# Optimization experiments

Measured on AMD Instinct MI355X. Metric: run time of the kernel, lower is better.

Reference implementation:

```python
import jax, jax.numpy as jnp
import numpy as np

HIDDEN = 1024
NUM_HEADS = 4
HEAD_DIM = HIDDEN // NUM_HEADS
SCALE = HEAD_DIM ** -0.5
EPS = 1e-5


def setup_inputs() -> dict:
    key = jax.random.key(0)
    ks = jax.random.split(key, 8)
    B, S, D = 4, 2048, HIDDEN
    x = jax.random.normal(ks[0], (B, S, D), dtype=jnp.float32)
    attention_mask = jnp.ones((B, S), dtype=jnp.int32)
    init = 1.0 / np.sqrt(D)
    Wq = jax.random.uniform(ks[1], (D, D), jnp.float32, -init, init)
    Wk = jax.random.uniform(ks[2], (D, D), jnp.float32, -init, init)
    Wv = jax.random.uniform(ks[3], (D, D), jnp.float32, -init, init)
    Wo = jax.random.uniform(ks[4], (D, D), jnp.float32, -init, init)
    bo = jax.random.uniform(ks[5], (D,), jnp.float32, -init, init)
    gamma = jnp.ones((D,), dtype=jnp.float32)
    beta = jnp.zeros((D,), dtype=jnp.float32)
    return {"x": x, "attention_mask": attention_mask, "Wq": Wq, "Wk": Wk,
            "Wv": Wv, "Wo": Wo, "bo": bo, "gamma": gamma, "beta": beta}


def reference(x, attention_mask, Wq, Wk, Wv, Wo, bo, gamma, beta):
    # Linear layers: y = x @ W^T (torch nn.Linear convention), no bias for q/k/v
    q = jnp.einsum('bsd,ed->bse', x, Wq)
    k = jnp.einsum('bsd,ed->bse', x, Wk)
    v = jnp.einsum('bsd,ed->bse', x, Wv)
    # Full-width attention (module never splits heads), scale = head_dim^-0.5
    scores = jnp.einsum('bqd,bkd->bqk', q, k) * SCALE  # [B,S,S]
    mask = attention_mask[:, None, :]  # [B,1,S]
    scores = jnp.where(mask == 0, jnp.float32(-1e9), scores)
    attn = jax.nn.softmax(scores, axis=-1)
    ctx = jnp.einsum('bqk,bkd->bqd', attn, v)
    out = jnp.einsum('bsd,ed->bse', ctx, Wo) + bo
    # residual + LayerNorm
    h = out + x
    mu = jnp.mean(h, axis=-1, keepdims=True)
    var = jnp.mean(jnp.square(h - mu), axis=-1, keepdims=True)
    return (h - mu) * jax.lax.rsqrt(var + EPS) * gamma + beta
```

## Files before the change

### kernel.cpp

```cpp
#include <hip/hip_runtime.h>

typedef __bf16 bf16;
typedef __bf16 bf16x8 __attribute__((ext_vector_type(8)));
typedef __bf16 bf16x4 __attribute__((ext_vector_type(4)));
typedef float floatx4 __attribute__((ext_vector_type(4)));

#define HIDDEN 1024
#define SEQ 2048
#define BATCH 4
#define ATT_SCALE 0.0625f
#define LN_EPS 1e-5f
#define WW (HIDDEN * HIDDEN)

__device__ __forceinline__ void gload_lds16(const void* g, void* l) {
    __builtin_amdgcn_global_load_lds(
        (const __attribute__((address_space(1))) unsigned int*)g,
        (__attribute__((address_space(3))) unsigned int*)l, 16, 0, 0);
}

#define GBAR() asm volatile("s_barrier" ::: "memory")
#define LGKM0() asm volatile("s_waitcnt lgkmcnt(0)" ::: "memory")
#define VMC(N) asm volatile("s_waitcnt vmcnt(" #N ")" ::: "memory")
#define MFMA(a, b, c) __builtin_amdgcn_mfma_f32_16x16x32_bf16(a, b, c, 0, 0, 0)
#define MFMA8(a, b, c) __builtin_amdgcn_mfma_f32_16x16x32_fp8_fp8(a, b, c, 0, 0, 0)

__device__ __forceinline__ unsigned char to_fp8(float f) {
    return (unsigned char)(__builtin_amdgcn_cvt_pk_fp8_f32(f, 0.0f, 0, 0) & 0xff);
}
__device__ __forceinline__ unsigned int to_fp8x2(float a, float b) {
    return __builtin_amdgcn_cvt_pk_fp8_f32(a, b, 0, 0) & 0xffff;
}

__global__ void cvt_f32_bf16(const float* __restrict__ in, bf16* __restrict__ out, int n4) {
    int i = blockIdx.x * blockDim.x + threadIdx.x;
    if (i >= n4) return;
    float4 v = ((const float4*)in)[i];
    bf16x4 o;
    o[0] = (bf16)v.x; o[1] = (bf16)v.y; o[2] = (bf16)v.z; o[3] = (bf16)v.w;
    ((bf16x4*)out)[i] = o;
}

__global__ void cvt_f32_fp8(const float* __restrict__ in, unsigned char* __restrict__ out, int n8) {
    int i = blockIdx.x * blockDim.x + threadIdx.x;
    if (i >= n8) return;
    float4 v0 = ((const float4*)in)[i * 2];
    float4 v1 = ((const float4*)in)[i * 2 + 1];
    unsigned int lo = to_fp8x2(v0.x, v0.y) | (to_fp8x2(v0.z, v0.w) << 16);
    unsigned int hi = to_fp8x2(v1.x, v1.y) | (to_fp8x2(v1.z, v1.w) << 16);
    ((uint2*)out)[i] = make_uint2(lo, hi);
}

__global__ void transpose_w3(const float* __restrict__ s0, const float* __restrict__ s1,
                             const float* __restrict__ s2,
                             bf16* __restrict__ d0p, bf16* __restrict__ d1p, bf16* __restrict__ d2p) {
    const float* in = (blockIdx.z == 0) ? s0 : (blockIdx.z == 1) ? s1 : s2;
    bf16* out = (blockIdx.z == 0) ? d0p : (blockIdx.z == 1) ? d1p : d2p;
    __shared__ __attribute__((aligned(16))) bf16 tile[64][72];
    const int d0 = blockIdx.x * 64;
    const int f0 = blockIdx.y * 64;
    const int t = threadIdx.x;
    const int r = t >> 4;
    const int c = (t & 15) * 4;
#pragma unroll
    for (int i = 0; i < 4; ++i) {
        float4 v = *(const float4*)&in[(long)(f0 + r + i * 16) * HIDDEN + d0 + c];
        bf16x4 b;
        b[0] = (bf16)v.x; b[1] = (bf16)v.y; b[2] = (bf16)v.z; b[3] = (bf16)v.w;
        *(bf16x4*)&tile[r + i * 16][c] = b;
    }
    __syncthreads();
#pragma unroll
    for (int i = 0; i < 4; ++i) {
        const int dr = r + i * 16;
        bf16x4 o;
#pragma unroll
        for (int j = 0; j < 4; ++j) o[j] = tile[c + j][dr];
        *(bf16x4*)&out[(long)(d0 + dr) * HIDDEN + f0 + c] = o;
    }
}

template <int MODE>
__global__ __launch_bounds__(512, 2)
void gemm8p(const bf16* A, const bf16* Bw, void* __restrict__ Cout,
            int lda, int ldb, int ldc, int K, float scale,
            long sA, long sB, long sC, int zmod) {
    __shared__ __attribute__((aligned(16))) char lds[131072];

    const int gx = gridDim.x;
    const int nblk = gx * gridDim.y;
    const int bid = blockIdx.y * gx + blockIdx.x;
    const int cpx = nblk >> 3;
    const int sbid = (nblk & 7) ? bid : (bid & 7) * cpx + (bid >> 3);
    const int bx = sbid % gx, by = sbid / gx;

    const int z = blockIdx.z;
    const int mat = z % zmod, ks = z / zmod;
    const char* Ab = (const char*)(A + (long)mat * sA + (long)ks * K);
    const char* Bb = (const char*)(Bw + (long)mat * sB + (long)ks * K);
    const long lda2 = lda * 2L, ldb2 = ldb * 2L;

    const int t = threadIdx.x;
    const int lane = t & 63;
    const int w = t >> 6;
    const int wm = w >> 2;
    const int wn = w & 3;
    const int l15 = lane & 15;
    const int l4 = lane >> 4;

    const int row0 = by * 256;
    const int col0 = bx * 256;

    const int sc = ((((t & 3) - ((t >> 3) & 3)) & 3) << 4);
    const char* aS[2];
    const char* bS[2];
#pragma unroll
    for (int uu = 0; uu < 2; ++uu) {
        aS[uu] = Ab + (long)(row0 + uu * 128 + (t >> 2)) * lda2 + sc;
        bS[uu] = Bb + (long)(col0 + uu * 128 + (t >> 2)) * ldb2 + sc;
    }

    auto STAGE = [&](char* dstu, const char* const* sp, long koff) {
        gload_lds16(sp[0] + koff, dstu + t * 16);
        gload_lds16(sp[1] + koff, dstu + 8192 + t * 16);
    };

    floatx4 acc[8][4] = {};
    const int nk = K / 64;

    STAGE(lds + 0,     aS, 0);
    STAGE(lds + 16384, bS, 0);
    STAGE(lds + 32768, aS, 64);
    STAGE(lds + 49152, bS, 64);
    VMC(4);
    GBAR();

    for (int tt = 0; tt < nk; ++tt) {
        const char* cb = lds + (tt & 1) * 65536;
        char* nb = lds + ((tt & 1) ^ 1) * 65536;
        const long nko = (long)((tt + 1 < nk) ? tt + 1 : nk - 1) * 128;

        auto RDA = [&](int kk, int m) {
            int lr = wm * 128 + m * 16 + l15;
            return *(const bf16x8*)(cb + kk * 32768 + lr * 64 + ((((lr >> 1) + l4) & 3) << 4));
        };
        auto RDB = [&](int kk, int n) {
            int lr = wn * 64 + n * 16 + l15;
            return *(const bf16x8*)(cb + 16384 + kk * 32768 + lr * 64 + ((((lr >> 1) + l4) & 3) << 4));
        };

        bf16x8 a[4], b0[4], b1[4];

#pragma unroll
        for (int m = 0; m < 4; ++m) a[m] = RDA(0, m);
#pragma unroll
        for (int n = 0; n < 4; ++n) b0[n] = RDB(0, n);
        STAGE(nb + 0, aS, nko);
        GBAR();
        LGKM0();
        __builtin_amdgcn_s_setprio(1);
#pragma unroll
        for (int m = 0; m < 4; ++m)
#pragma unroll
            for (int n = 0; n < 4; ++n) acc[m][n] = MFMA(a[m], b0[n], acc[m][n]);
        __builtin_amdgcn_s_setprio(0);
        GBAR();

#pragma unroll
        for (int m = 0; m < 4; ++m) a[m] = RDA(0, 4 + m);
        STAGE(nb + 16384, bS, nko);
        GBAR();
        LGKM0();
        __builtin_amdgcn_s_setprio(1);
#pragma unroll
        for (int m = 0; m < 4; ++m)
#pragma unroll
            for (int n = 0; n < 4; ++n) acc[4 + m][n] = MFMA(a[m], b0[n], acc[4 + m][n]);
        __builtin_amdgcn_s_setprio(0);
        VMC(4);
        GBAR();

#pragma unroll
        for (int m = 0; m < 4; ++m) a[m] = RDA(1, m);
#pragma unroll
        for (int n = 0; n < 4; ++n) b1[n] = RDB(1, n);
        STAGE(nb + 32768, aS, nko + 64);
        GBAR();
        LGKM0();
        __builtin_amdgcn_s_setprio(1);
#pragma unroll
        for (int m = 0; m < 4; ++m)
#pragma unroll
            for (int n = 0; n < 4; ++n) acc[m][n] = MFMA(a[m], b1[n], acc[m][n]);
        __builtin_amdgcn_s_setprio(0);
        GBAR();

#pragma unroll
        for (int m = 0; m < 4; ++m) a[m] = RDA(1, 4 + m);
        STAGE(nb + 49152, bS, nko + 64);
        GBAR();
        LGKM0();
        __builtin_amdgcn_s_setprio(1);
#pragma unroll
        for (int m = 0; m < 4; ++m)
#pragma unroll
            for (int n = 0; n < 4; ++n) acc[4 + m][n] = MFMA(a[m], b1[n], acc[4 + m][n]);
        __builtin_amdgcn_s_setprio(0);
        VMC(4);
        GBAR();
    }
    VMC(0);

    const int rq = l4 * 4;
    if constexpr (MODE == 0) {
        bf16* C = ((bf16*)Cout) + (long)z * sC;
#pragma unroll
        for (int m = 0; m < 8; ++m)
#pragma unroll
            for (int i = 0; i < 4; ++i) {
                long gr = row0 + wm * 128 + m * 16 + rq + i;
#pragma unroll
                for (int n = 0; n < 4; ++n) {
                    int gc = col0 + wn * 64 + n * 16 + l15;
                    C[gr * ldc + gc] = (bf16)(acc[m][n][i] * scale);
                }
            }
    } else {
        float* C = (float*)Cout + (long)z * sC;
#pragma unroll
        for (int m = 0; m < 8; ++m)
#pragma unroll
            for (int i = 0; i < 4; ++i) {
                long gr = row0 + wm * 128 + m * 16 + rq + i;
#pragma unroll
                for (int n = 0; n < 4; ++n) {
                    int gc = col0 + wn * 64 + n * 16 + l15;
                    C[gr * ldc + gc] = acc[m][n][i];
                }
            }
    }
}

template <int MODE>
__global__ __launch_bounds__(512, 2)
void gemmf8(const unsigned char* A, const unsigned char* Bw, void* __restrict__ Cout,
            int lda, int ldb, int ldc, int K, float scale,
            long sA, long sB, long sC, int zmod) {
    __shared__ __attribute__((aligned(16))) char lds[65536];

    const int gx = gridDim.x;
    const int nblk = gx * gridDim.y;
    const int bid = blockIdx.y * gx + blockIdx.x;
    const int cpx = nblk >> 3;
    const int sbid = (nblk & 7) ? bid : (bid & 7) * cpx + (bid >> 3);
    const int bx = sbid % gx, by = sbid / gx;

    const int z = blockIdx.z;
    const int mat = z % zmod, ks = z / zmod;
    const unsigned char* Ab = A + (long)mat * sA + (long)ks * K;
    const unsigned char* Bb = Bw + (long)mat * sB + (long)ks * K;

    const int t = threadIdx.x;
    const int lane = t & 63;
    const int w = t >> 6;
    const int wm = w >> 2;
    const int wn = w & 3;
    const int l15 = lane & 15;
    const int l4 = lane >> 4;

    const int row0 = by * 256;
    const int col0 = bx * 256;

    const int r_st = t >> 1;
    const int u_g = ((t & 1) + (t >> 3)) & 1;
    const unsigned char* aSrc = Ab + (long)(row0 + r_st) * lda + u_g * 16;
    const unsigned char* bSrc = Bb + (long)(col0 + r_st) * ldb + u_g * 16;
    const int ld16 = t * 16;

    auto STAGE = [&](int slot, long koff) {
        char* base = lds + slot * 32768;
        gload_lds16(aSrc + koff,      base + ld16);
        gload_lds16(aSrc + koff + 32, base + 8192 + ld16);
        gload_lds16(bSrc + koff,      base + 16384 + ld16);
        gload_lds16(bSrc + koff + 32, base + 24576 + ld16);
    };

    floatx4 acc[8][4] = {};
    const int nk = K / 64;

    STAGE(0, 0);
    VMC(0);
    GBAR();

    for (int s = 0; s < nk; ++s) {
        const char* sb = lds + (s & 1) * 32768;
        const long pko = (long)((s + 1 < nk) ? s + 1 : nk - 1) * 64;
        STAGE((s + 1) & 1, pko);

        auto RD = [&](const char* unit, int r) {
            int addr = r * 32 + ((((l4 >> 1) + (r >> 2)) & 1) << 4) + ((l4 & 1) << 3);
            return *(const long*)(unit + addr);
        };

        long a[8], b[4];
#pragma unroll
        for (int n = 0; n < 4; ++n) b[n] = RD(sb + 16384, wn * 64 + n * 16 + l15);
#pragma unroll
        for (int m = 0; m < 8; ++m) a[m] = RD(sb, wm * 128 + m * 16 + l15);
        __builtin_amdgcn_s_setprio(1);
#pragma unroll
        for (int m = 0; m < 8; ++m)
#pragma unroll
            for (int n = 0; n < 4; ++n) acc[m][n] = MFMA8(a[m], b[n], acc[m][n]);
        __builtin_amdgcn_s_setprio(0);
#pragma unroll
        for (int n = 0; n < 4; ++n) b[n] = RD(sb + 24576, wn * 64 + n * 16 + l15);
#pragma unroll
        for (int m = 0; m < 8; ++m) a[m] = RD(sb + 8192, wm * 128 + m * 16 + l15);
        __builtin_amdgcn_s_setprio(1);
#pragma unroll
        for (int m = 0; m < 8; ++m)
#pragma unroll
            for (int n = 0; n < 4; ++n) acc[m][n] = MFMA8(a[m], b[n], acc[m][n]);
        __builtin_amdgcn_s_setprio(0);

        VMC(0);
        GBAR();
    }

    const int rq = l4 * 4;
    if constexpr (MODE == 0) {
        bf16* C = ((bf16*)Cout) + (long)z * sC;
#pragma unroll
        for (int m = 0; m < 8; ++m)
#pragma unroll
            for (int i = 0; i < 4; ++i) {
                long gr = row0 + wm * 128 + m * 16 + rq + i;
#pragma unroll
                for (int n = 0; n < 4; ++n) {
                    int gc = col0 + wn * 64 + n * 16 + l15;
                    C[gr * ldc + gc] = (bf16)(acc[m][n][i] * scale);
                }
            }
    } else {
        unsigned char* C = ((unsigned char*)Cout) + (long)z * sC;
#pragma unroll
        for (int m = 0; m < 8; ++m)
#pragma unroll
            for (int i = 0; i < 4; ++i) {
                long gr = row0 + wm * 128 + m * 16 + rq + i;
#pragma unroll
                for (int n = 0; n < 4; ++n) {
                    int gc = col0 + wn * 64 + n * 16 + l15;
                    C[gr * ldc + gc] = to_fp8(acc[m][n][i] * scale);
                }
            }
    }
}

__global__ void reduce_wgc(const float* __restrict__ p, unsigned char* __restrict__ out) {
    int i = blockIdx.x * blockDim.x + threadIdx.x;
    int e = i * 4;
    int mat = e >> 20;
    int local = e & (WW - 1);
    float4 s = *(const float4*)(p + (long)mat * WW + local);
#pragma unroll
    for (int ksp = 1; ksp < 4; ++ksp) {
        float4 a = *(const float4*)(p + (long)(ksp * 2 + mat) * WW + local);
        s.x += a.x; s.y += a.y; s.z += a.z; s.w += a.w;
    }
    unsigned int pk = to_fp8x2(s.x * 64.f, s.y * 64.f) | (to_fp8x2(s.z * 64.f, s.w * 64.f) << 16);
    *(unsigned int*)&out[e] = pk;
}

__global__ void softmax_rows(const bf16* __restrict__ S, unsigned char* __restrict__ P,
                             const int* __restrict__ mask) {
    const int b = blockIdx.y;
    const int row = blockIdx.x;
    const bf16* srow = S + ((long)b * SEQ + row) * SEQ;
    unsigned char* prow = P + ((long)b * SEQ + row) * SEQ;
    const int* mrow = mask + b * SEQ;
    const int t = threadIdx.x;

    bf16x8 sv = *(const bf16x8*)&srow[t * 8];
    int4 m0 = ((const int4*)mrow)[t * 2];
    int4 m1 = ((const int4*)mrow)[t * 2 + 1];
    int mk[8] = {m0.x, m0.y, m0.z, m0.w, m1.x, m1.y, m1.z, m1.w};

    float v[8];
    float mx = -1e30f;
#pragma unroll
    for (int j = 0; j < 8; ++j) {
        float s = (float)sv[j];
        if (mk[j] == 0) s = -1e9f;
        v[j] = s;
        mx = fmaxf(mx, s);
    }
    __shared__ float redm[4], reds[4];
#pragma unroll
    for (int off = 32; off > 0; off >>= 1) mx = fmaxf(mx, __shfl_down(mx, off));
    if ((t & 63) == 0) redm[t >> 6] = mx;
    __syncthreads();
    mx = fmaxf(fmaxf(redm[0], redm[1]), fmaxf(redm[2], redm[3]));

    float sum = 0.f;
#pragma unroll
    for (int j = 0; j < 8; ++j) {
        v[j] = __expf(v[j] - mx);
        sum += v[j];
    }
#pragma unroll
    for (int off = 32; off > 0; off >>= 1) sum += __shfl_down(sum, off);
    if ((t & 63) == 0) reds[t >> 6] = sum;
    __syncthreads();
    sum = reds[0] + reds[1] + reds[2] + reds[3];
    float inv = 256.0f / sum;

    unsigned int lo = to_fp8x2(v[0] * inv, v[1] * inv) | (to_fp8x2(v[2] * inv, v[3] * inv) << 16);
    unsigned int hi = to_fp8x2(v[4] * inv, v[5] * inv) | (to_fp8x2(v[6] * inv, v[7] * inv) << 16);
    *(uint2*)&prow[t * 8] = make_uint2(lo, hi);
}

__global__ void transpose_v8(const unsigned char* __restrict__ yv, unsigned char* __restrict__ out) {
    __shared__ unsigned char tile[64][68];
    const int z = blockIdx.z;
    const unsigned char* ib = yv + (long)z * SEQ * 2048 + 1024;
    unsigned char* ob = out + (long)z * (long)HIDDEN * SEQ;
    const int d0 = blockIdx.x * 64;
    const int s0 = blockIdx.y * 64;
    const int t = threadIdx.x;
    const int r = t >> 4;
    const int c = (t & 15) * 4;
#pragma unroll
    for (int i = 0; i < 4; ++i) {
        uchar4 v = *(const uchar4*)&ib[(long)(s0 + r + i * 16) * 2048 + d0 + c];
        *(uchar4*)&tile[r + i * 16][c] = v;
    }
    __syncthreads();
#pragma unroll
    for (int i = 0; i < 4; ++i) {
        const int dr = r + i * 16;
        uchar4 o;
        o.x = tile[c + 0][dr]; o.y = tile[c + 1][dr];
        o.z = tile[c + 2][dr]; o.w = tile[c + 3][dr];
        *(uchar4*)&ob[(long)(d0 + dr) * SEQ + s0 + c] = o;
    }
}

__global__ void layernorm_out(const bf16* __restrict__ pp, const float* __restrict__ x,
                              const float* __restrict__ bo, const float* __restrict__ gamma,
                              const float* __restrict__ beta, float* __restrict__ out) {
    const long row = blockIdx.x;
    const int b = (int)(row >> 11);
    const int s = (int)(row & 2047);
    const bf16* r0 = pp + ((long)b * SEQ + s) * HIDDEN;
    const bf16* r1 = r0 + 4L * SEQ * HIDDEN;
    const int t = threadIdx.x;

    bf16x4 a0 = ((const bf16x4*)r0)[t];
    bf16x4 a1 = ((const bf16x4*)r1)[t];
    float4 xv = ((const float4*)(x + row * HIDDEN))[t];
    float4 bv = ((const float4*)bo)[t];
    float4 v;
    v.x = (float)a0[0] + (float)a1[0] + bv.x + xv.x;
    v.y = (float)a0[1] + (float)a1[1] + bv.y + xv.y;
    v.z = (float)a0[2] + (float)a1[2] + bv.z + xv.z;
    v.w = (float)a0[3] + (float)a1[3] + bv.w + xv.w;

    float ssum = v.x + v.y + v.z + v.w;
    float sq = v.x * v.x + v.y * v.y + v.z * v.z + v.w * v.w;
    __shared__ float rs[4], rq[4];
#pragma unroll
    for (int off = 32; off > 0; off >>= 1) {
        ssum += __shfl_down(ssum, off);
        sq += __shfl_down(sq, off);
    }
    if ((t & 63) == 0) { rs[t >> 6] = ssum; rq[t >> 6] = sq; }
    __syncthreads();
    ssum = rs[0] + rs[1] + rs[2] + rs[3];
    sq = rq[0] + rq[1] + rq[2] + rq[3];
    float mu = ssum * (1.0f / HIDDEN);
    float var = sq * (1.0f / HIDDEN) - mu * mu;
    float rinv = rsqrtf(var + LN_EPS);
    float4 g = ((const float4*)gamma)[t];
    float4 bt = ((const float4*)beta)[t];
    float4 o;
    o.x = (v.x - mu) * rinv * g.x + bt.x;
    o.y = (v.y - mu) * rinv * g.y + bt.y;
    o.z = (v.z - mu) * rinv * g.z + bt.z;
    o.w = (v.w - mu) * rinv * g.w + bt.w;
    ((float4*)(out + row * HIDDEN))[t] = o;
}

extern "C" void kernel_launch(void* const* d_in, const int* in_sizes, int n_in,
                              void* d_out, int out_size, void* d_ws, size_t ws_size,
                              hipStream_t stream) {
    const float* x     = (const float*)d_in[0];
    const int*   mask  = (const int*)d_in[1];
    const float* Wq    = (const float*)d_in[2];
    const float* Wk    = (const float*)d_in[3];
    const float* Wv    = (const float*)d_in[4];
    const float* Wo    = (const float*)d_in[5];
    const float* bo    = (const float*)d_in[6];
    const float* gamma = (const float*)d_in[7];
    const float* beta  = (const float*)d_in[8];
    float* out = (float*)d_out;

    char* ws = (char*)d_ws;
    const long MB = 1024L * 1024L;
    unsigned char* xb8  = (unsigned char*)(ws + 0 * MB);
    unsigned char* yv8  = (unsigned char*)(ws + 8 * MB);
    unsigned char* vt8  = (unsigned char*)(ws + 24 * MB);
    unsigned char* wgc8 = (unsigned char*)(ws + 32 * MB);
    bf16* wkT = (bf16*)(ws + 34 * MB);
    bf16* wo  = (bf16*)(ws + 36 * MB);
    bf16* wqT = (bf16*)(ws + 38 * MB);
    bf16* wvT = (bf16*)(ws + 40 * MB);
    bf16* S   = (bf16*)(ws + 42 * MB);
    float* wgcp = (float*)(ws + 42 * MB);
    bf16* pp  = (bf16*)(ws + 42 * MB);
    unsigned char* P8 = (unsigned char*)(ws + 74 * MB);

    const int BS = BATCH * SEQ;
    dim3 blk256(256), blk512(512);

    cvt_f32_fp8<<<dim3(BS * HIDDEN / 8 / 256), blk256, 0, stream>>>(x, xb8, BS * HIDDEN / 8);
    cvt_f32_bf16<<<dim3(WW / 4 / 256), blk256, 0, stream>>>(Wo, wo, WW / 4);
    transpose_w3<<<dim3(16, 16, 3), blk256, 0, stream>>>(Wq, Wk, Wv, wqT, wkT, wvT);

    gemm8p<4><<<dim3(1024 / 256, 1024 / 256, 8), blk512, 0, stream>>>(
        wkT, wqT, wgcp, HIDDEN, HIDDEN, HIDDEN, 256, 1.0f,
        (long)WW, (long)WW, (long)WW, 2);
    reduce_wgc<<<dim3(2 * WW / 4 / 256), blk256, 0, stream>>>(wgcp, wgc8);

    gemmf8<1><<<dim3(2048 / 256, BS / 256, 1), blk512, 0, stream>>>(
        xb8, wgc8, yv8, HIDDEN, HIDDEN, 2048, HIDDEN, 1.0f / 64.0f, 0, 0, 0, 1);

    transpose_v8<<<dim3(HIDDEN / 64, SEQ / 64, BATCH), blk256, 0, stream>>>(yv8, vt8);

    gemmf8<0><<<dim3(SEQ / 256, SEQ / 256, BATCH), blk512, 0, stream>>>(
        yv8, xb8, S, 2048, HIDDEN, SEQ, HIDDEN, ATT_SCALE,
        (long)SEQ * 2048, (long)SEQ * HIDDEN, (long)SEQ * SEQ, 4);

    softmax_rows<<<dim3(SEQ, BATCH), blk256, 0, stream>>>(S, P8, mask);

    gemmf8<0><<<dim3(HIDDEN / 256, SEQ / 256, 8), blk512, 0, stream>>>(
        P8, vt8, pp, SEQ, SEQ, HIDDEN, 1024, 1.0f / 256.0f,
        (long)SEQ * SEQ, (long)HIDDEN * SEQ, (long)SEQ * HIDDEN, 4);

    layernorm_out<<<dim3(BS), blk256, 0, stream>>>(pp, x, bo, gamma, beta, out);
}
```

Baseline: 169.7 us.

## Shrink fp8 GEMM tiles to 256x128 with 4 waves; fuse weight prep; bf16 partials

```diff
diff --git a/kernel.cpp b/kernel.cpp
--- a/kernel.cpp
+++ b/kernel.cpp
@@ -29,15 +29,6 @@
 }
 __device__ __forceinline__ unsigned int to_fp8x2(float a, float b) {
     return __builtin_amdgcn_cvt_pk_fp8_f32(a, b, 0, 0) & 0xffff;
-}
-
-__global__ void cvt_f32_bf16(const float* __restrict__ in, bf16* __restrict__ out, int n4) {
-    int i = blockIdx.x * blockDim.x + threadIdx.x;
-    if (i >= n4) return;
-    float4 v = ((const float4*)in)[i];
-    bf16x4 o;
-    o[0] = (bf16)v.x; o[1] = (bf16)v.y; o[2] = (bf16)v.z; o[3] = (bf16)v.w;
-    ((bf16x4*)out)[i] = o;
 }
 
 __global__ void cvt_f32_fp8(const float* __restrict__ in, unsigned char* __restrict__ out, int n8) {
@@ -50,17 +41,29 @@
     ((uint2*)out)[i] = make_uint2(lo, hi);
 }
 
-__global__ void transpose_w3(const float* __restrict__ s0, const float* __restrict__ s1,
-                             const float* __restrict__ s2,
-                             bf16* __restrict__ d0p, bf16* __restrict__ d1p, bf16* __restrict__ d2p) {
-    const float* in = (blockIdx.z == 0) ? s0 : (blockIdx.z == 1) ? s1 : s2;
-    bf16* out = (blockIdx.z == 0) ? d0p : (blockIdx.z == 1) ? d1p : d2p;
-    __shared__ __attribute__((aligned(16))) bf16 tile[64][72];
+__global__ void transpose_w4(const float* __restrict__ s0, const float* __restrict__ s1,
+                             const float* __restrict__ s2, const float* __restrict__ s3,
+                             bf16* __restrict__ d0p, bf16* __restrict__ d1p,
+                             bf16* __restrict__ d2p, bf16* __restrict__ d3p) {
+    const int zz = blockIdx.z;
+    const float* in = (zz == 0) ? s0 : (zz == 1) ? s1 : (zz == 2) ? s2 : s3;
+    bf16* out = (zz == 0) ? d0p : (zz == 1) ? d1p : (zz == 2) ? d2p : d3p;
     const int d0 = blockIdx.x * 64;
     const int f0 = blockIdx.y * 64;
     const int t = threadIdx.x;
     const int r = t >> 4;
     const int c = (t & 15) * 4;
+    if (zz == 3) {
+#pragma unroll
+        for (int i = 0; i < 4; ++i) {
+            float4 v = *(const float4*)&in[(long)(f0 + r + i * 16) * HIDDEN + d0 + c];
+            bf16x4 b;
+            b[0] = (bf16)v.x; b[1] = (bf16)v.y; b[2] = (bf16)v.z; b[3] = (bf16)v.w;
+            *(bf16x4*)&out[(long)(f0 + r + i * 16) * HIDDEN + d0 + c] = b;
+        }
+        return;
+    }
+    __shared__ __attribute__((aligned(16))) bf16 tile[64][72];
 #pragma unroll
     for (int i = 0; i < 4; ++i) {
         float4 v = *(const float4*)&in[(long)(f0 + r + i * 16) * HIDDEN + d0 + c];
@@ -211,41 +214,26 @@
     VMC(0);
 
     const int rq = l4 * 4;
-    if constexpr (MODE == 0) {
-        bf16* C = ((bf16*)Cout) + (long)z * sC;
-#pragma unroll
-        for (int m = 0; m < 8; ++m)
-#pragma unroll
-            for (int i = 0; i < 4; ++i) {
-                long gr = row0 + wm * 128 + m * 16 + rq + i;
-#pragma unroll
-                for (int n = 0; n < 4; ++n) {
-                    int gc = col0 + wn * 64 + n * 16 + l15;
-                    C[gr * ldc + gc] = (bf16)(acc[m][n][i] * scale);
-                }
+    bf16* C = ((bf16*)Cout) + (long)z * sC;
+#pragma unroll
+    for (int m = 0; m < 8; ++m)
+#pragma unroll
+        for (int i = 0; i < 4; ++i) {
+            long gr = row0 + wm * 128 + m * 16 + rq + i;
+#pragma unroll
+            for (int n = 0; n < 4; ++n) {
+                int gc = col0 + wn * 64 + n * 16 + l15;
+                C[gr * ldc + gc] = (bf16)(acc[m][n][i] * scale);
             }
-    } else {
-        float* C = (float*)Cout + (long)z * sC;
-#pragma unroll
-        for (int m = 0; m < 8; ++m)
-#pragma unroll
-            for (int i = 0; i < 4; ++i) {
-                long gr = row0 + wm * 128 + m * 16 + rq + i;
-#pragma unroll
-                for (int n = 0; n < 4; ++n) {
-                    int gc = col0 + wn * 64 + n * 16 + l15;
-                    C[gr * ldc + gc] = acc[m][n][i];
-                }
-            }
-    }
+        }
 }
 
 template <int MODE>
-__global__ __launch_bounds__(512, 2)
+__global__ __launch_bounds__(256, 3)
 void gemmf8(const unsigned char* A, const unsigned char* Bw, void* __restrict__ Cout,
             int lda, int ldb, int ldc, int K, float scale,
             long sA, long sB, long sC, int zmod) {
-    __shared__ __attribute__((aligned(16))) char lds[65536];
+    __shared__ __attribute__((aligned(16))) char lds[49152];
 
     const int gx = gridDim.x;
     const int nblk = gx * gridDim.y;
@@ -262,26 +250,29 @@
     const int t = threadIdx.x;
     const int lane = t & 63;
     const int w = t >> 6;
-    const int wm = w >> 2;
-    const int wn = w & 3;
+    const int wm = w >> 1;
+    const int wn = w & 1;
     const int l15 = lane & 15;
     const int l4 = lane >> 4;
 
     const int row0 = by * 256;
-    const int col0 = bx * 256;
+    const int col0 = bx * 128;
 
     const int r_st = t >> 1;
     const int u_g = ((t & 1) + (t >> 3)) & 1;
-    const unsigned char* aSrc = Ab + (long)(row0 + r_st) * lda + u_g * 16;
-    const unsigned char* bSrc = Bb + (long)(col0 + r_st) * ldb + u_g * 16;
+    const unsigned char* aS0 = Ab + (long)(row0 + r_st) * lda + u_g * 16;
+    const unsigned char* aS1 = Ab + (long)(row0 + 128 + r_st) * lda + u_g * 16;
+    const unsigned char* bS0 = Bb + (long)(col0 + r_st) * ldb + u_g * 16;
     const int ld16 = t * 16;
 
     auto STAGE = [&](int slot, long koff) {
-        char* base = lds + slot * 32768;
-        gload_lds16(aSrc + koff,      base + ld16);
-        gload_lds16(aSrc + koff + 32, base + 8192 + ld16);
-        gload_lds16(bSrc + koff,      base + 16384 + ld16);
-        gload_lds16(bSrc + koff + 32, base + 24576 + ld16);
+        char* base = lds + slot * 24576;
+        gload_lds16(aS0 + koff,      base + ld16);
+        gload_lds16(aS1 + koff,      base + 4096 + ld16);
+        gload_lds16(aS0 + koff + 32, base + 8192 + ld16);
+        gload_lds16(aS1 + koff + 32, base + 12288 + ld16);
+        gload_lds16(bS0 + koff,      base + 16384 + ld16);
+        gload_lds16(bS0 + koff + 32, base + 20480 + ld16);
     };
 
     floatx4 acc[8][4] = {};
@@ -292,7 +283,7 @@
     GBAR();
 
     for (int s = 0; s < nk; ++s) {
-        const char* sb = lds + (s & 1) * 32768;
+        const char* sb = lds + (s & 1) * 24576;
         const long pko = (long)((s + 1 < nk) ? s + 1 : nk - 1) * 64;
         STAGE((s + 1) & 1, pko);
 
@@ -313,7 +304,7 @@
             for (int n = 0; n < 4; ++n) acc[m][n] = MFMA8(a[m], b[n], acc[m][n]);
         __builtin_amdgcn_s_setprio(0);
 #pragma unroll
-        for (int n = 0; n < 4; ++n) b[n] = RD(sb + 24576, wn * 64 + n * 16 + l15);
+        for (int n = 0; n < 4; ++n) b[n] = RD(sb + 20480, wn * 64 + n * 16 + l15);
 #pragma unroll
         for (int m = 0; m < 8; ++m) a[m] = RD(sb + 8192, wm * 128 + m * 16 + l15);
         __builtin_amdgcn_s_setprio(1);
@@ -357,18 +348,18 @@
     }
 }
 
-__global__ void reduce_wgc(const float* __restrict__ p, unsigned char* __restrict__ out) {
+__global__ void reduce_wgc(const bf16* __restrict__ p, unsigned char* __restrict__ out) {
     int i = blockIdx.x * blockDim.x + threadIdx.x;
     int e = i * 4;
     int mat = e >> 20;
     int local = e & (WW - 1);
-    float4 s = *(const float4*)(p + (long)mat * WW + local);
-#pragma unroll
-    for (int ksp = 1; ksp < 4; ++ksp) {
-        float4 a = *(const float4*)(p + (long)(ksp * 2 + mat) * WW + local);
-        s.x += a.x; s.y += a.y; s.z += a.z; s.w += a.w;
-    }
-    unsigned int pk = to_fp8x2(s.x * 64.f, s.y * 64.f) | (to_fp8x2(s.z * 64.f, s.w * 64.f) << 16);
+    float s0 = 0, s1 = 0, s2 = 0, s3 = 0;
+#pragma unroll
+    for (int ksp = 0; ksp < 4; ++ksp) {
+        bf16x4 a = *(const bf16x4*)(p + (long)(ksp * 2 + mat) * WW + local);
+        s0 += (float)a[0]; s1 += (float)a[1]; s2 += (float)a[2]; s3 += (float)a[3];
+    }
+    unsigned int pk = to_fp8x2(s0 * 64.f, s1 * 64.f) | (to_fp8x2(s2 * 64.f, s3 * 64.f) << 16);
     *(unsigned int*)&out[e] = pk;
 }
 
@@ -516,7 +507,7 @@
     bf16* wqT = (bf16*)(ws + 38 * MB);
     bf16* wvT = (bf16*)(ws + 40 * MB);
     bf16* S   = (bf16*)(ws + 42 * MB);
-    float* wgcp = (float*)(ws + 42 * MB);
+    bf16* wgcp = (bf16*)(ws + 42 * MB);
     bf16* pp  = (bf16*)(ws + 42 * MB);
     unsigned char* P8 = (unsigned char*)(ws + 74 * MB);
 
@@ -524,26 +515,25 @@
     dim3 blk256(256), blk512(512);
 
     cvt_f32_fp8<<<dim3(BS * HIDDEN / 8 / 256), blk256, 0, stream>>>(x, xb8, BS * HIDDEN / 8);
-    cvt_f32_bf16<<<dim3(WW / 4 / 256), blk256, 0, stream>>>(Wo, wo, WW / 4);
-    transpose_w3<<<dim3(16, 16, 3), blk256, 0, stream>>>(Wq, Wk, Wv, wqT, wkT, wvT);
-
-    gemm8p<4><<<dim3(1024 / 256, 1024 / 256, 8), blk512, 0, stream>>>(
+    transpose_w4<<<dim3(16, 16, 4), blk256, 0, stream>>>(Wq, Wk, Wv, Wo, wqT, wkT, wvT, wo);
+
+    gemm8p<0><<<dim3(1024 / 256, 1024 / 256, 8), blk512, 0, stream>>>(
         wkT, wqT, wgcp, HIDDEN, HIDDEN, HIDDEN, 256, 1.0f,
         (long)WW, (long)WW, (long)WW, 2);
     reduce_wgc<<<dim3(2 * WW / 4 / 256), blk256, 0, stream>>>(wgcp, wgc8);
 
-    gemmf8<1><<<dim3(2048 / 256, BS / 256, 1), blk512, 0, stream>>>(
+    gemmf8<1><<<dim3(2048 / 128, BS / 256, 1), blk256, 0, stream>>>(
         xb8, wgc8, yv8, HIDDEN, HIDDEN, 2048, HIDDEN, 1.0f / 64.0f, 0, 0, 0, 1);
 
     transpose_v8<<<dim3(HIDDEN / 64, SEQ / 64, BATCH), blk256, 0, stream>>>(yv8, vt8);
 
-    gemmf8<0><<<dim3(SEQ / 256, SEQ / 256, BATCH), blk512, 0, stream>>>(
+    gemmf8<0><<<dim3(SEQ / 128, SEQ / 256, BATCH), blk256, 0, stream>>>(
         yv8, xb8, S, 2048, HIDDEN, SEQ, HIDDEN, ATT_SCALE,
         (long)SEQ * 2048, (long)SEQ * HIDDEN, (long)SEQ * SEQ, 4);
 
     softmax_rows<<<dim3(SEQ, BATCH), blk256, 0, stream>>>(S, P8, mask);
 
-    gemmf8<0><<<dim3(HIDDEN / 256, SEQ / 256, 8), blk512, 0, stream>>>(
+    gemmf8<0><<<dim3(HIDDEN / 128, SEQ / 256, 8), blk256, 0, stream>>>(
         P8, vt8, pp, SEQ, SEQ, HIDDEN, 1024, 1.0f / 256.0f,
         (long)SEQ * SEQ, (long)HIDDEN * SEQ, (long)SEQ * HIDDEN, 4);
 
```

Measured after the change: 188.4 us. 11.0% more time.
